# Kernel optimization log

Measured on AMD Instinct MI355X. Metric: run time of the kernel, lower is better.

Reference implementation:

```python
import jax, jax.numpy as jnp
import numpy as np

OFFSET_FP32 = np.uint32(1064828928)  # L-mul exponent-bias correction constant for float32


def lmul_matmul(A, B):
    """Approximate A @ B (m,n)x(n,p) via integer-add-as-multiply on float bit patterns.

    Torch ref adds bit patterns in int64 then truncates with .to(torch.uint32),
    i.e. arithmetic mod 2**32 -- identical to plain uint32 wraparound addition,
    so we stay in uint32 and avoid needing x64 mode.
    """
    Au = jax.lax.bitcast_convert_type(A, jnp.uint32)          # (m, n)
    Bu = jax.lax.bitcast_convert_type(B, jnp.uint32)          # (n, p)
    prod_bits = Au[:, :, None] + Bu[None, :, :] - OFFSET_FP32  # (m, n, p), wraps mod 2^32
    prod = jax.lax.bitcast_convert_type(prod_bits, jnp.float32)
    return prod.sum(axis=1)                                    # (m, p)


def setup_inputs() -> dict:
    key = jax.random.key(0)
    k1, k2, k3 = jax.random.split(key, 3)
    m, n, p = 256, 512, 512
    x = jax.random.normal(k1, (m, n), dtype=jnp.float32)
    bound = 1.0 / np.sqrt(n)  # kaiming_uniform(a=sqrt(5)) -> U(-1/sqrt(fan_in), 1/sqrt(fan_in))
    weight = jax.random.uniform(k2, (p, n), dtype=jnp.float32, minval=-bound, maxval=bound)
    bias = jax.random.uniform(k3, (p,), dtype=jnp.float32, minval=-bound, maxval=bound)
    return {"x": x, "weight": weight, "bias": bias}


def reference(x, weight, bias):
    out = lmul_matmul(x, weight.T)
    return out + bias
```

## Files before the change

### kernel.cpp

```cpp
#include <hip/hip_runtime.h>
#include <stdint.h>


#define OFFSET_FP32 1064828928u

constexpr int M = 256;
constexpr int N = 512;
constexpr int P = 512;

constexpr int BM = 4;
constexpr int BP = 128;
constexpr int KT = 64;

__global__ __launch_bounds__(256) void lmul_linear_kernel(
    const uint32_t* __restrict__ xb,
    const uint32_t* __restrict__ wb,
    const float*    __restrict__ bias,
    float*          __restrict__ out)
{
    __shared__ uint32_t Bs[KT][BP + 1];

    const int tid     = threadIdx.x;
    const int p_local = tid & (BP - 1);
    const int m_local = tid >> 7;

    const int p0 = blockIdx.x * BP;
    const int m0 = blockIdx.y * BM + m_local * 2;
    const int p  = p0 + p_local;

    const uint32_t* xrow0 = xb + (size_t)m0 * N;
    const uint32_t* xrow1 = xb + (size_t)(m0 + 1) * N;

    float acc0 = 0.0f, acc1 = 0.0f;

    const int wk  = tid & (KT - 1);
    const int wp4 = tid >> 6;

    for (int k0 = 0; k0 < N; k0 += KT) {
        #pragma unroll
        for (int j = 0; j < BP / 4; ++j) {
            const int pp = wp4 + j * 4;
            Bs[wk][pp] = wb[(size_t)(p0 + pp) * N + (k0 + wk)] - OFFSET_FP32;
        }
        __syncthreads();

        #pragma unroll 16
        for (int kk = 0; kk < KT; ++kk) {
            const uint32_t b  = Bs[kk][p_local];
            const uint32_t a0 = xrow0[k0 + kk];
            const uint32_t a1 = xrow1[k0 + kk];
            acc0 += __uint_as_float(a0 + b);
            acc1 += __uint_as_float(a1 + b);
        }
        __syncthreads();
    }

    const float bv = bias[p];
    out[(size_t)m0 * P + p]       = acc0 + bv;
    out[(size_t)(m0 + 1) * P + p] = acc1 + bv;
}

extern "C" void kernel_launch(void* const* d_in, const int* in_sizes, int n_in,
                              void* d_out, int out_size, void* d_ws, size_t ws_size,
                              hipStream_t stream) {
    const uint32_t* xb   = (const uint32_t*)d_in[0];
    const uint32_t* wb   = (const uint32_t*)d_in[1];
    const float*    bias = (const float*)d_in[2];
    float*          out  = (float*)d_out;

    dim3 grid(P / BP, M / BM);
    dim3 block(256);
    lmul_linear_kernel<<<grid, block, 0, stream>>>(xb, wb, bias, out);
}
```

Baseline: 72.68 us.

## Vectorize W tile loads, swizzle shared layout, and prefetch next tile into registers

After: 70.73 us. 1.03x faster.

```diff
diff --git a/kernel.cpp b/kernel.cpp
--- a/kernel.cpp
+++ b/kernel.cpp
@@ -10,54 +10,73 @@
 
 constexpr int BM = 4;
 constexpr int BP = 128;
-constexpr int KT = 64;
+constexpr int KT = 128;
 
-__global__ __launch_bounds__(256) void lmul_linear_kernel(
+__global__ __launch_bounds__(512) void lmul_linear_kernel(
     const uint32_t* __restrict__ xb,
     const uint32_t* __restrict__ wb,
     const float*    __restrict__ bias,
     float*          __restrict__ out)
 {
-    __shared__ uint32_t Bs[KT][BP + 1];
+    __shared__ uint32_t Bs[BP * KT];
 
     const int tid     = threadIdx.x;
     const int p_local = tid & (BP - 1);
     const int m_local = tid >> 7;
 
     const int p0 = blockIdx.x * BP;
-    const int m0 = blockIdx.y * BM + m_local * 2;
-    const int p  = p0 + p_local;
+    const int m  = blockIdx.y * BM + m_local;
 
-    const uint32_t* xrow0 = xb + (size_t)m0 * N;
-    const uint32_t* xrow1 = xb + (size_t)(m0 + 1) * N;
+    const uint32_t* xrow  = xb + (size_t)m * N;
+    const uint32_t* wbase = wb + (size_t)p0 * N;
 
-    float acc0 = 0.0f, acc1 = 0.0f;
+    const int sg  = tid & 31;
+    const int sr0 = tid >> 5;
 
-    const int wk  = tid & (KT - 1);
-    const int wp4 = tid >> 6;
+    uint4 stage[8];
 
-    for (int k0 = 0; k0 < N; k0 += KT) {
+    auto load_tile = [&](int k0) {
         #pragma unroll
-        for (int j = 0; j < BP / 4; ++j) {
-            const int pp = wp4 + j * 4;
-            Bs[wk][pp] = wb[(size_t)(p0 + pp) * N + (k0 + wk)] - OFFSET_FP32;
+        for (int ps = 0; ps < 8; ++ps) {
+            const int pp = sr0 + ps * 16;
+            stage[ps] = *(const uint4*)(wbase + (size_t)pp * N + k0 + sg * 4);
         }
+    };
+    auto store_tile = [&]() {
+        #pragma unroll
+        for (int ps = 0; ps < 8; ++ps) {
+            const int pp = sr0 + ps * 16;
+            const int pg = sg ^ (pp & 7);
+            uint4 v = stage[ps];
+            v.x -= OFFSET_FP32; v.y -= OFFSET_FP32;
+            v.z -= OFFSET_FP32; v.w -= OFFSET_FP32;
+            *(uint4*)&Bs[pp * KT + pg * 4] = v;
+        }
+    };
+
+    float acc0 = 0.f, acc1 = 0.f, acc2 = 0.f, acc3 = 0.f;
+
+    load_tile(0);
+    for (int t = 0; t < N / KT; ++t) {
         __syncthreads();
+        store_tile();
+        __syncthreads();
+        if (t + 1 < N / KT) load_tile((t + 1) * KT);
 
-        #pragma unroll 16
-        for (int kk = 0; kk < KT; ++kk) {
-            const uint32_t b  = Bs[kk][p_local];
-            const uint32_t a0 = xrow0[k0 + kk];
-            const uint32_t a1 = xrow1[k0 + kk];
-            acc0 += __uint_as_float(a0 + b);
-            acc1 += __uint_as_float(a1 + b);
+        const int k0 = t * KT;
+        #pragma unroll 8
+        for (int j = 0; j < KT / 4; ++j) {
+            const uint4 b = *(const uint4*)&Bs[p_local * KT + ((j ^ (p_local & 7)) * 4)];
+            const uint4 a = *(const uint4*)(xrow + k0 + j * 4);
+            acc0 += __uint_as_float(a.x + b.x);
+            acc1 += __uint_as_float(a.y + b.y);
+            acc2 += __uint_as_float(a.z + b.z);
+            acc3 += __uint_as_float(a.w + b.w);
         }
-        __syncthreads();
     }
 
-    const float bv = bias[p];
-    out[(size_t)m0 * P + p]       = acc0 + bv;
-    out[(size_t)(m0 + 1) * P + p] = acc1 + bv;
+    const int p = p0 + p_local;
+    out[(size_t)m * P + p] = (acc0 + acc1) + (acc2 + acc3) + bias[p];
 }
 
 extern "C" void kernel_launch(void* const* d_in, const int* in_sizes, int n_in,
@@ -69,6 +88,6 @@
     float*          out  = (float*)d_out;
 
     dim3 grid(P / BP, M / BM);
-    dim3 block(256);
+    dim3 block(512);
     lmul_linear_kernel<<<grid, block, 0, stream>>>(xb, wb, bias, out);
 }
```

## Split-K with atomics, 4-row register tiling, vectorized swizzled LDS loads

Applied to the files above, without the earlier changes.

New measurement: 64.70 us (median of 2 runs). -11.0%, faster.

```diff
diff --git a/kernel.cpp b/kernel.cpp
--- a/kernel.cpp
+++ b/kernel.cpp
@@ -8,9 +8,11 @@
 constexpr int N = 512;
 constexpr int P = 512;
 
-constexpr int BM = 4;
 constexpr int BP = 128;
-constexpr int KT = 64;
+constexpr int BM = 8;
+constexpr int TM = 4;
+constexpr int KS = 4;
+constexpr int KT = N / KS;
 
 __global__ __launch_bounds__(256) void lmul_linear_kernel(
     const uint32_t* __restrict__ xb,
@@ -18,46 +20,71 @@
     const float*    __restrict__ bias,
     float*          __restrict__ out)
 {
-    __shared__ uint32_t Bs[KT][BP + 1];
+    __shared__ uint32_t Bs[BP * KT];
 
     const int tid     = threadIdx.x;
     const int p_local = tid & (BP - 1);
-    const int m_local = tid >> 7;
+    const int m_quad  = __builtin_amdgcn_readfirstlane(tid >> 7);
 
-    const int p0 = blockIdx.x * BP;
-    const int m0 = blockIdx.y * BM + m_local * 2;
-    const int p  = p0 + p_local;
+    const int p0 = blockIdx.y * BP;
+    const int m0 = blockIdx.x * BM + m_quad * TM;
+    const int k0 = blockIdx.z * KT;
 
-    const uint32_t* xrow0 = xb + (size_t)m0 * N;
-    const uint32_t* xrow1 = xb + (size_t)(m0 + 1) * N;
+    const int sg = tid & 31;
+    const int sr = tid >> 5;
+    const uint32_t* wbase = wb + (size_t)p0 * N + k0;
+    #pragma unroll
+    for (int j = 0; j < 16; ++j) {
+        const int pp = sr + j * 8;
+        uint4 v = *(const uint4*)(wbase + (size_t)pp * N + sg * 4);
+        v.x -= OFFSET_FP32; v.y -= OFFSET_FP32;
+        v.z -= OFFSET_FP32; v.w -= OFFSET_FP32;
+        const int g = sg ^ (pp & 7);
+        *(uint4*)&Bs[pp * KT + g * 4] = v;
+    }
+    __syncthreads();
 
-    float acc0 = 0.0f, acc1 = 0.0f;
+    const uint32_t* xr0 = xb + (size_t)(m0 + 0) * N + k0;
+    const uint32_t* xr1 = xb + (size_t)(m0 + 1) * N + k0;
+    const uint32_t* xr2 = xb + (size_t)(m0 + 2) * N + k0;
+    const uint32_t* xr3 = xb + (size_t)(m0 + 3) * N + k0;
 
-    const int wk  = tid & (KT - 1);
-    const int wp4 = tid >> 6;
+    float acc[TM][4] = {};
+    const uint32_t* brow = &Bs[p_local * KT];
+    const int rot = p_local & 7;
 
-    for (int k0 = 0; k0 < N; k0 += KT) {
-        #pragma unroll
-        for (int j = 0; j < BP / 4; ++j) {
-            const int pp = wp4 + j * 4;
-            Bs[wk][pp] = wb[(size_t)(p0 + pp) * N + (k0 + wk)] - OFFSET_FP32;
-        }
-        __syncthreads();
-
-        #pragma unroll 16
-        for (int kk = 0; kk < KT; ++kk) {
-            const uint32_t b  = Bs[kk][p_local];
-            const uint32_t a0 = xrow0[k0 + kk];
-            const uint32_t a1 = xrow1[k0 + kk];
-            acc0 += __uint_as_float(a0 + b);
-            acc1 += __uint_as_float(a1 + b);
-        }
-        __syncthreads();
+    #pragma unroll 8
+    for (int j = 0; j < KT / 4; ++j) {
+        const uint4 b  = *(const uint4*)&brow[(j ^ rot) * 4];
+        const uint4 a0 = *(const uint4*)(xr0 + j * 4);
+        const uint4 a1 = *(const uint4*)(xr1 + j * 4);
+        const uint4 a2 = *(const uint4*)(xr2 + j * 4);
+        const uint4 a3 = *(const uint4*)(xr3 + j * 4);
+        acc[0][0] += __uint_as_float(a0.x + b.x);
+        acc[0][1] += __uint_as_float(a0.y + b.y);
+        acc[0][2] += __uint_as_float(a0.z + b.z);
+        acc[0][3] += __uint_as_float(a0.w + b.w);
+        acc[1][0] += __uint_as_float(a1.x + b.x);
+        acc[1][1] += __uint_as_float(a1.y + b.y);
+        acc[1][2] += __uint_as_float(a1.z + b.z);
+        acc[1][3] += __uint_as_float(a1.w + b.w);
+        acc[2][0] += __uint_as_float(a2.x + b.x);
+        acc[2][1] += __uint_as_float(a2.y + b.y);
+        acc[2][2] += __uint_as_float(a2.z + b.z);
+        acc[2][3] += __uint_as_float(a2.w + b.w);
+        acc[3][0] += __uint_as_float(a3.x + b.x);
+        acc[3][1] += __uint_as_float(a3.y + b.y);
+        acc[3][2] += __uint_as_float(a3.z + b.z);
+        acc[3][3] += __uint_as_float(a3.w + b.w);
     }
 
-    const float bv = bias[p];
-    out[(size_t)m0 * P + p]       = acc0 + bv;
-    out[(size_t)(m0 + 1) * P + p] = acc1 + bv;
+    const int p  = p0 + p_local;
+    const float bv = (k0 == 0) ? bias[p] : 0.0f;
+    #pragma unroll
+    for (int r = 0; r < TM; ++r) {
+        const float s = (acc[r][0] + acc[r][1]) + (acc[r][2] + acc[r][3]) + bv;
+        atomicAdd(&out[(size_t)(m0 + r) * P + p], s);
+    }
 }
 
 extern "C" void kernel_launch(void* const* d_in, const int* in_sizes, int n_in,
@@ -68,7 +95,9 @@
     const float*    bias = (const float*)d_in[2];
     float*          out  = (float*)d_out;
 
-    dim3 grid(P / BP, M / BM);
+    hipMemsetAsync(d_out, 0, (size_t)out_size * sizeof(float), stream);
+
+    dim3 grid(M / BM, P / BP, KS);
     dim3 block(256);
     lmul_linear_kernel<<<grid, block, 0, stream>>>(xb, wb, bias, out);
 }
```
